# Performance work log

Hardware: AMD Instinct MI355X
Metric: run time of the kernel (lower is better)

Reference implementation:

```python
import jax, jax.numpy as jnp
import numpy as np

N = 10000        # nodes
E = 160000       # edges (before self-loops)
NFEAT = 256
NHID = 128
H = 4            # heads
NCLASS = 40
NLAYERS = 2
DT = 1.0
ALPHA = 1.0
GAMMA = 1.0
NEG_SLOPE = 0.2  # GATConv leaky_relu slope


def setup_inputs() -> dict:
    key = jax.random.key(0)
    ks = jax.random.split(key, 12)

    def glorot(k, shape):
        fan_in, fan_out = shape[-1], shape[0]
        lim = (6.0 / (fan_in + fan_out)) ** 0.5
        return jax.random.uniform(k, shape, jnp.float32, -lim, lim)

    return {
        "x": jax.random.normal(ks[0], (N, NFEAT), jnp.float32),
        "edge_index": jax.random.randint(ks[1], (2, E), 0, N, jnp.int64),
        "enc_w": glorot(ks[2], (NHID, NFEAT)),
        "enc_b": jnp.zeros((NHID,), jnp.float32),
        "res_w": glorot(ks[3], (H * NHID, NHID)),
        "res_b": jnp.zeros((H * NHID,), jnp.float32),
        "gat_w": glorot(ks[4], (H * NHID, NHID)),
        "att_src": glorot(ks[5], (H, NHID)) * 0.1,
        "att_dst": glorot(ks[6], (H, NHID)) * 0.1,
        "gat_b": jnp.zeros((H * NHID,), jnp.float32),
        "dec_w": glorot(ks[7], (NCLASS, NHID)),
        "dec_b": jnp.zeros((NCLASS,), jnp.float32),
    }


def _gat_conv(x, src, dst, gat_w, att_src, att_dst, gat_b):
    # x: [N, NHID] -> per-head features [N, H, C]
    xh = (x @ gat_w.T).reshape(N, H, NHID)
    a_src = jnp.sum(xh * att_src[None], axis=-1)  # [N, H]
    a_dst = jnp.sum(xh * att_dst[None], axis=-1)  # [N, H]
    e = jax.nn.leaky_relu(a_src[src] + a_dst[dst], NEG_SLOPE)  # [E', H]
    # segment softmax over incoming edges of each destination node
    m = jax.ops.segment_max(e, dst, num_segments=N)            # [N, H]
    e = jnp.exp(e - m[dst])
    s = jax.ops.segment_sum(e, dst, num_segments=N)            # [N, H]
    alpha = e / s[dst]                                          # [E', H]
    msg = xh[src] * alpha[:, :, None]                           # [E', H, C]
    out = jax.ops.segment_sum(msg, dst, num_segments=N)         # [N, H, C]
    return out.reshape(N, H * NHID) + gat_b


def reference(x, edge_index, enc_w, enc_b, res_w, res_b, gat_w,
              att_src, att_dst, gat_b, dec_w, dec_b):
    # add self-loops (GATConv default)
    loop = jnp.arange(N, dtype=edge_index.dtype)
    src = jnp.concatenate([edge_index[0], loop])
    dst = jnp.concatenate([edge_index[1], loop])

    Y = jax.nn.relu(x @ enc_w.T + enc_b)  # [N, NHID]
    X = Y
    for _ in range(NLAYERS):
        conv = _gat_conv(X, src, dst, gat_w, att_src, att_dst, gat_b)  # [N, H*NHID]
        res = X @ res_w.T + res_b                                       # [N, H*NHID]
        # faithful to .view(n_nodes, -1, nheads).mean(-1): [N, NHID, H] -> mean over heads axis
        z = jax.nn.elu(conv + res).reshape(N, NHID, H).mean(axis=-1)    # [N, NHID]
        Y = Y + DT * (z - ALPHA * Y - GAMMA * X)
        X = X + DT * Y
    return X @ dec_w.T + dec_b  # [N, NCLASS]
```

## Files before the change

### kernel.cpp

```cpp
#include <hip/hip_runtime.h>
#include <math.h>

#define NN 10000
#define EE 160000
#define EP 170000
#define NFEAT 256
#define NHID 128
#define NH 4
#define HF 512
#define NCLASS 40
#define FCOLS 1088

typedef __attribute__((ext_vector_type(8))) short bf8;
typedef __attribute__((ext_vector_type(8))) unsigned short u16x8;
typedef __attribute__((ext_vector_type(4))) float f4;

__device__ __forceinline__ float leaky02(float x) { return x >= 0.0f ? x : 0.2f * x; }

__device__ __forceinline__ unsigned short f2bf(float f) {
    unsigned u = __builtin_bit_cast(unsigned, f);
    unsigned r = (u + 0x7FFF + ((u >> 16) & 1)) >> 16;
    return (unsigned short)r;
}
__device__ __forceinline__ float bf2f(unsigned short h) {
    return __builtin_bit_cast(float, (unsigned)h << 16);
}

__device__ __forceinline__ int swz(int row, int c) {
    return ((((c >> 3) ^ (row & 7)) << 3) | (c & 7));
}

__device__ __forceinline__ void gl_lds16(const unsigned short* g, unsigned short* l)
{
    __builtin_amdgcn_global_load_lds(
        (const __attribute__((address_space(1))) unsigned int*)g,
        (__attribute__((address_space(3))) unsigned int*)l, 16, 0, 0);
}

#define C_X   2560000
#define C_EW  (C_X + 32768)
#define C_FW  (C_EW + 131072)
#define CVT_B  1330
#define ATTW_B (CVT_B + 8)
#define TOT_B  (ATTW_B + 166)

__global__ __launch_bounds__(256)
void fused0_k(const float* __restrict__ x, const float* __restrict__ enc_w,
              const float* __restrict__ gat_w, const float* __restrict__ res_w,
              const float* __restrict__ att_src, const float* __restrict__ att_dst,
              const float* __restrict__ res_b, const float* __restrict__ gat_b,
              const int* __restrict__ ei,
              unsigned short* __restrict__ xhi, unsigned short* __restrict__ ewhi,
              unsigned short* __restrict__ fwhi,
              float* __restrict__ biasRG, int* __restrict__ cnt)
{
    int bId = blockIdx.x;
    int t = threadIdx.x;
    if (bId < CVT_B) {
        int iu = bId * 256 + t;
        int i = iu * 8;
        const float* src = nullptr; unsigned short* ph; int j, row, c, Kd;
        if (i < C_X)       { j = i;        src = x;     ph = xhi;
                             row = j >> 8; c = j & 255; Kd = 256; }
        else if (i < C_EW) { j = i - C_X;  src = enc_w; ph = ewhi;
                             row = j >> 8; c = j & 255; Kd = 256; }
        else               { j = i - C_EW; ph = fwhi;
                             row = j >> 7; c = j & 127; Kd = 128; }
        float4 v0, v1;
        if (src) { v0 = *(const float4*)(src + j); v1 = *(const float4*)(src + j + 4); }
        else {
            const float* s2 = (j < 65536) ? (gat_w + j) : (res_w + j - 65536);
            v0 = *(const float4*)s2; v1 = *(const float4*)(s2 + 4);
        }
        float vv[8] = {v0.x, v0.y, v0.z, v0.w, v1.x, v1.y, v1.z, v1.w};
        unsigned short hs[8];
#pragma unroll
        for (int k = 0; k < 8; ++k) hs[k] = f2bf(vv[k]);
        int outp = row * Kd + swz(row, c);
        *(u16x8*)(ph + outp) = *(u16x8*)hs;
    } else if (bId < ATTW_B) {
        __shared__ float sm[256];
        int b = bId - CVT_B;
        int is_dst = b >> 2, h = b & 3;
        const float* att = is_dst ? att_dst : att_src;
        int k = t & 127, half = t >> 7;
        float s = 0.0f;
#pragma unroll 4
        for (int c = half * 64; c < half * 64 + 64; ++c)
            s = fmaf(gat_w[(size_t)(h * 128 + c) * 128 + k], att[h * 128 + c], s);
        sm[t] = s;
        __syncthreads();
        if (t < 128) {
            float v = sm[t] + sm[t + 128];
            int R = 1024 + is_dst * 4 + h;
            fwhi[(size_t)R * 128 + swz(R, k)] = f2bf(v);
        }
        for (int i = b * 896 + t; i < (b + 1) * 896; i += 256)
            fwhi[1032 * 128 + i] = 0;
        if (b < 2) {
            int c = b * 256 + t;
            biasRG[c] = res_b[c] + gat_b[c];
        }
    } else {
        for (int e = (bId - ATTW_B) * 256 + t; e < EP; e += (TOT_B - ATTW_B) * 256) {
            int d = (e < EE) ? ei[EE + e] : (e - EE);
            atomicAdd(&cnt[d], 1);
        }
    }
}

template<int MODE, int KTILES, int MERGE>
__global__ __launch_bounds__(256)
void gemm3_k(const unsigned short* __restrict__ A, const unsigned short* __restrict__ B,
             const float* __restrict__ bias,
             unsigned short* __restrict__ outH, unsigned short* __restrict__ outL,
             float* __restrict__ a_src, float* __restrict__ a_dst, int M,
             const int* __restrict__ ei, const int* __restrict__ cnt,
             int* __restrict__ row_ptr, int* __restrict__ cursor, int* __restrict__ csr)
{
    constexpr int K = KTILES * 128;
    __shared__ __align__(16) unsigned short smem[2 * 64 * 128];
    const int tid = threadIdx.x;

    if (MERGE && blockIdx.y == gridDim.y - 1) {
        if (MERGE == 1) {
            if (blockIdx.x != 0) return;
            int* smi = (int*)smem;
            int i0 = tid * 40, i1 = min(i0 + 40, NN);
            int part = 0;
            for (int i = i0; i < i1; ++i) part += cnt[i];
            smi[tid] = part;
            __syncthreads();
            for (int off = 1; off < 256; off <<= 1) {
                int v = (tid >= off) ? smi[tid - off] : 0;
                __syncthreads();
                smi[tid] += v;
                __syncthreads();
            }
            int run = smi[tid] - part;
            for (int i = i0; i < i1; ++i) { row_ptr[i] = run; run += cnt[i]; }
            if (tid == 255) row_ptr[NN] = run;
        } else {
            int stride = gridDim.x * 256;
            for (int e = blockIdx.x * 256 + tid; e < EP; e += stride) {
                int s, d;
                if (e < EE) { s = ei[e]; d = ei[EE + e]; } else { s = e - EE; d = s; }
                int pos = row_ptr[d] + atomicAdd(&cursor[d], 1);
                csr[pos] = s;
            }
        }
        return;
    }

    unsigned short* sA = smem;
    unsigned short* sB = smem + 8192;

    const int lane = tid & 63, wv = tid >> 6;
    const int wr = (wv >> 1) * 32, wc = (wv & 1) * 32;
    const int bm = blockIdx.x * 64, bn = blockIdx.y * 64;
    const int r16 = lane & 15, q4 = lane >> 4;

    f4 acc[2][2];
#pragma unroll
    for (int i = 0; i < 2; ++i)
#pragma unroll
        for (int j = 0; j < 2; ++j) acc[i][j] = (f4){0.f, 0.f, 0.f, 0.f};

    const int ra0 = wr + r16;
    const int rb0 = wc + r16;

    for (int kt = 0; kt < KTILES; ++kt) {
        if (kt) __syncthreads();
#pragma unroll
        for (int j = 0; j < 4; ++j) {
            int i = tid + j * 256;
            int row = i >> 4, u = i & 15;
            int arow = min(bm + row, M - 1);
            size_t ga = (size_t)arow * K + kt * 128 + u * 8;
            size_t gb = (size_t)(bn + row) * K + kt * 128 + u * 8;
            int lb = (wv * 64 + j * 256) * 8;
            gl_lds16(A + ga, sA + lb);
            gl_lds16(B + gb, sB + lb);
        }
        __syncthreads();

#pragma unroll
        for (int ks = 0; ks < 4; ++ks) {
            int u = ks * 4 + q4;
            int oa0 = ra0 * 128 + ((u ^ (ra0 & 7)) * 8);
            int ob0 = rb0 * 128 + ((u ^ (rb0 & 7)) * 8);
            int oa1 = oa0 + 16 * 128;
            int ob1 = ob0 + 16 * 128;
            bf8 A0 = *(const bf8*)(sA + oa0);
            bf8 A1 = *(const bf8*)(sA + oa1);
            bf8 B0 = *(const bf8*)(sB + ob0);
            bf8 B1 = *(const bf8*)(sB + ob1);

            acc[0][0] = __builtin_amdgcn_mfma_f32_16x16x32_bf16(A0, B0, acc[0][0], 0, 0, 0);
            acc[0][1] = __builtin_amdgcn_mfma_f32_16x16x32_bf16(A0, B1, acc[0][1], 0, 0, 0);
            acc[1][0] = __builtin_amdgcn_mfma_f32_16x16x32_bf16(A1, B0, acc[1][0], 0, 0, 0);
            acc[1][1] = __builtin_amdgcn_mfma_f32_16x16x32_bf16(A1, B1, acc[1][1], 0, 0, 0);
        }
    }

    const int rbase = q4 * 4;

    if (MODE == 2 && bn >= 1024) {
#pragma unroll
        for (int i = 0; i < 2; ++i)
#pragma unroll
            for (int j = 0; j < 2; ++j)
#pragma unroll
                for (int r = 0; r < 4; ++r) {
                    int row = bm + wr + i * 16 + rbase + r;
                    int col = bn + wc + j * 16 + r16;
                    if (row >= M || col >= 1032) continue;
                    float v = acc[i][j][r];
                    int h = col - 1024;
                    if (h < 4) a_src[row * 4 + h] = v;
                    else       a_dst[row * 4 + h - 4] = v;
                }
        return;
    }

    __syncthreads();
    float* sC = (float*)smem;
#pragma unroll
    for (int i = 0; i < 2; ++i)
#pragma unroll
        for (int j = 0; j < 2; ++j)
#pragma unroll
            for (int r = 0; r < 4; ++r)
                sC[(wr + i * 16 + rbase + r) * 65 + (wc + j * 16 + r16)] = acc[i][j][r];
    __syncthreads();

    int row = tid >> 2, seg = tid & 3, c0 = seg * 16;
    int grow = bm + row;
    if (grow < M) {
        float v[16];
#pragma unroll
        for (int k = 0; k < 16; ++k) v[k] = sC[row * 65 + c0 + k];

        if (MODE == 1) {
            unsigned short hs[16];
#pragma unroll
            for (int k = 0; k < 16; ++k)
                hs[k] = f2bf(fmaxf(v[k] + bias[bn + c0 + k], 0.0f));
#pragma unroll
            for (int uu = 0; uu < 2; ++uu) {
                int ug = (bn + c0) / 8 + uu;
                int pu = ug ^ (grow & 7);
                *(u16x8*)(outH + (size_t)grow * 128 + pu * 8) = *(u16x8*)(hs + uu * 8);
            }
        } else {
            if (bn < 512) {
                unsigned short hs[16];
#pragma unroll
                for (int k = 0; k < 16; ++k) hs[k] = f2bf(v[k]);
                *(u16x8*)(outH + (size_t)grow * 512 + bn + c0)     = *(u16x8*)hs;
                *(u16x8*)(outH + (size_t)grow * 512 + bn + c0 + 8) = *(u16x8*)(hs + 8);
            } else {
                unsigned short hs[16];
#pragma unroll
                for (int k = 0; k < 16; ++k) hs[k] = f2bf(v[k] + bias[bn - 512 + c0 + k]);
                *(u16x8*)(outL + (size_t)grow * 512 + (bn - 512) + c0)     = *(u16x8*)hs;
                *(u16x8*)(outL + (size_t)grow * 512 + (bn - 512) + c0 + 8) = *(u16x8*)(hs + 8);
            }
        }
    }
}

template<int DEC>
__global__ __launch_bounds__(256)
void agg_k(const int* __restrict__ row_ptr, const int* __restrict__ csr,
           const float* __restrict__ a_src, const float* __restrict__ a_dst,
           const unsigned short* __restrict__ xh_b, const unsigned short* __restrict__ resb,
           unsigned short* __restrict__ Xhi,
           const float* __restrict__ dec_w, const float* __restrict__ dec_b,
           float* __restrict__ out)
{
    __shared__ float sAcc[2][64][8];
    __shared__ float sSum[2][64];
    int tid = threadIdx.x;
    int wv = tid >> 6, lane = tid & 63;
    int pair = wv >> 1, half = wv & 1;
    int d = blockIdx.x * 2 + pair;
    int beg = row_ptr[d], end = row_ptr[d + 1];
    int len = end - beg;
    int h0 = (len + 1) >> 1;
    int eb = half ? (beg + h0) : beg;
    int en = half ? end : (beg + h0);
    int hl = lane >> 4;
    int cb = lane * 8;
    float ad = a_dst[d * 4 + hl];
    u16x8 rv = *(const u16x8*)(resb + (size_t)d * HF + cb);

    float acc[8];
#pragma unroll
    for (int k = 0; k < 8; ++k) acc[k] = 0.0f;
    float ssum = 0.0f;

    int e = eb;
    for (; e + 8 <= en; e += 8) {
        int sv[8]; float w[8]; u16x8 v[8];
#pragma unroll
        for (int q = 0; q < 8; ++q) sv[q] = csr[e + q];
#pragma unroll
        for (int q = 0; q < 8; ++q) v[q] = *(const u16x8*)(xh_b + (size_t)sv[q] * HF + cb);
#pragma unroll
        for (int q = 0; q < 8; ++q) {
            w[q] = __expf(leaky02(a_src[sv[q] * 4 + hl] + ad));
            ssum += w[q];
        }
#pragma unroll
        for (int q = 0; q < 8; ++q)
#pragma unroll
            for (int k = 0; k < 8; ++k) acc[k] = fmaf(w[q], bf2f(v[q][k]), acc[k]);
    }
    for (; e + 4 <= en; e += 4) {
        int sv[4]; float w[4]; u16x8 v[4];
#pragma unroll
        for (int q = 0; q < 4; ++q) sv[q] = csr[e + q];
#pragma unroll
        for (int q = 0; q < 4; ++q) v[q] = *(const u16x8*)(xh_b + (size_t)sv[q] * HF + cb);
#pragma unroll
        for (int q = 0; q < 4; ++q) {
            w[q] = __expf(leaky02(a_src[sv[q] * 4 + hl] + ad));
            ssum += w[q];
        }
#pragma unroll
        for (int q = 0; q < 4; ++q)
#pragma unroll
            for (int k = 0; k < 8; ++k) acc[k] = fmaf(w[q], bf2f(v[q][k]), acc[k]);
    }
    for (; e < en; ++e) {
        int s = csr[e];
        float w = __expf(leaky02(a_src[s * 4 + hl] + ad));
        ssum += w;
        u16x8 v = *(const u16x8*)(xh_b + (size_t)s * HF + cb);
#pragma unroll
        for (int k = 0; k < 8; ++k) acc[k] = fmaf(w, bf2f(v[k]), acc[k]);
    }

    if (half) {
        *(float4*)&sAcc[pair][lane][0] = make_float4(acc[0], acc[1], acc[2], acc[3]);
        *(float4*)&sAcc[pair][lane][4] = make_float4(acc[4], acc[5], acc[6], acc[7]);
        sSum[pair][lane] = ssum;
    }
    __syncthreads();

    float z0 = 0.0f, z1 = 0.0f;
    if (!half) {
#pragma unroll
        for (int k = 0; k < 8; ++k) acc[k] += sAcc[pair][lane][k];
        ssum += sSum[pair][lane];

        float inv = 1.0f / ssum;
        float uv[8];
#pragma unroll
        for (int k = 0; k < 8; ++k) {
            float v = fmaf(acc[k], inv, bf2f(rv[k]));
            uv[k] = (v > 0.0f) ? v : expm1f(v);
        }
        z0 = (uv[0] + uv[1] + uv[2] + uv[3]) * 0.25f;
        z1 = (uv[4] + uv[5] + uv[6] + uv[7]) * 0.25f;
        unsigned short h0b = f2bf(z0), h1b = f2bf(z1);
        int pos = swz(d, lane * 2);
        size_t idx = (size_t)d * NHID + pos;
        *(unsigned*)(Xhi + idx) = ((unsigned)h1b << 16) | h0b;
    }

    if (DEC) {
        __syncthreads();
        float* zbuf = &sAcc[0][0][0];
        if (!half) {
            zbuf[pair * 128 + lane * 2]     = z0;
            zbuf[pair * 128 + lane * 2 + 1] = z1;
        }
        __syncthreads();
        if (tid < 80) {
            int nd = tid >= 40;
            int cp = tid - nd * 40;
            const float* zr = zbuf + nd * 128;
            const float* wr = dec_w + cp * 128;
            float s = dec_b[cp];
#pragma unroll 8
            for (int c = 0; c < 128; ++c) s = fmaf(zr[c], wr[c], s);
            out[(size_t)(blockIdx.x * 2 + nd) * NCLASS + cp] = s;
        }
    }
}

extern "C" void kernel_launch(void* const* d_in, const int* in_sizes, int n_in,
                              void* d_out, int out_size, void* d_ws, size_t ws_size,
                              hipStream_t stream)
{
    const float* x       = (const float*)d_in[0];
    const int*   ei      = (const int*)d_in[1];
    const float* enc_w   = (const float*)d_in[2];
    const float* enc_b   = (const float*)d_in[3];
    const float* res_w   = (const float*)d_in[4];
    const float* res_b   = (const float*)d_in[5];
    const float* gat_w   = (const float*)d_in[6];
    const float* att_src = (const float*)d_in[7];
    const float* att_dst = (const float*)d_in[8];
    const float* gat_b   = (const float*)d_in[9];
    const float* dec_w   = (const float*)d_in[10];
    const float* dec_b   = (const float*)d_in[11];
    float* out = (float*)d_out;

    char* p = (char*)d_ws;
    auto alloc = [&](size_t bytes) -> void* {
        void* r = (void*)p;
        p += (bytes + 255) & ~(size_t)255;
        return r;
    };
    float* a_src  = (float*)alloc(40000 * 4);
    float* a_dst  = (float*)alloc(40000 * 4);
    float* biasRG = (float*)alloc(512 * 4);
    unsigned short* xh_b = (unsigned short*)alloc(5120000 * 2);
    unsigned short* resb = (unsigned short*)alloc(5120000 * 2);
    unsigned short* Xhi  = (unsigned short*)alloc(1280000 * 2);
    unsigned short* xhi  = (unsigned short*)alloc(2560000 * 2);
    unsigned short* ewhi = (unsigned short*)alloc(32768 * 2);
    unsigned short* fwhi = (unsigned short*)alloc(FCOLS * 128 * 2);
    int* row_ptr = (int*)alloc(10004 * 4);
    int* csr     = (int*)alloc(170000 * 4);
    char* zbase = p;
    int* cnt    = (int*)alloc(10000 * 4);
    int* cursor = (int*)alloc(10000 * 4);
    size_t zbytes = (size_t)(p - zbase);

    hipMemsetAsync(zbase, 0, zbytes, stream);

    fused0_k<<<TOT_B, 256, 0, stream>>>(
        x, enc_w, gat_w, res_w, att_src, att_dst, res_b, gat_b, ei,
        xhi, ewhi, fwhi, biasRG, cnt);

    gemm3_k<1, 2, 1><<<dim3(157, 3), 256, 0, stream>>>(
        xhi, ewhi, enc_b, Xhi, nullptr, nullptr, nullptr, NN,
        nullptr, cnt, row_ptr, nullptr, nullptr);

    gemm3_k<2, 1, 2><<<dim3(157, 18), 256, 0, stream>>>(
        Xhi, fwhi, biasRG, xh_b, resb, a_src, a_dst, NN,
        ei, nullptr, row_ptr, cursor, csr);
    agg_k<0><<<5000, 256, 0, stream>>>(row_ptr, csr, a_src, a_dst, xh_b, resb, Xhi,
                                       nullptr, nullptr, nullptr);

    gemm3_k<2, 1, 0><<<dim3(157, 17), 256, 0, stream>>>(
        Xhi, fwhi, biasRG, xh_b, resb, a_src, a_dst, NN,
        nullptr, nullptr, nullptr, nullptr, nullptr);
    agg_k<1><<<5000, 256, 0, stream>>>(row_ptr, csr, a_src, a_dst, xh_b, resb, Xhi,
                                       dec_w, dec_b, out);
}
```

Measured before the change: 223.3 us.

## Split aggregation per head across edge-groups and move decoder to MFMA GEMM

The aggregation kernel is reorganised so each block handles one head for four nodes: each wave's lanes cover four edge groups times 16 channel chunks, and the groups are combined with cross-lane shuffles instead of an LDS reduction between two half-waves. The decoder, previously a scalar per-block dot product fused into the last aggregation, becomes a separate bf16 MFMA GEMM launch reading a dec_w copy converted to bf16 in the prep kernel. This aims to remove block synchronisation and the slow scalar decode, at the cost of one extra launch and bf16 rounding of decoder weights. The same node's residual row and a_dst are now read by four different blocks, one per head.

Result: faster. 206.7 us (median of 2 runs) (-7.4%).

```diff
diff --git a/kernel.cpp b/kernel.cpp
--- a/kernel.cpp
+++ b/kernel.cpp
@@ -40,18 +40,20 @@
 #define C_X   2560000
 #define C_EW  (C_X + 32768)
 #define C_FW  (C_EW + 131072)
-#define CVT_B  1330
+#define C_DW  (C_FW + 5120)
+#define CVT_B  1333
 #define ATTW_B (CVT_B + 8)
 #define TOT_B  (ATTW_B + 166)
 
 __global__ __launch_bounds__(256)
 void fused0_k(const float* __restrict__ x, const float* __restrict__ enc_w,
               const float* __restrict__ gat_w, const float* __restrict__ res_w,
+              const float* __restrict__ dec_w,
               const float* __restrict__ att_src, const float* __restrict__ att_dst,
               const float* __restrict__ res_b, const float* __restrict__ gat_b,
               const int* __restrict__ ei,
               unsigned short* __restrict__ xhi, unsigned short* __restrict__ ewhi,
-              unsigned short* __restrict__ fwhi,
+              unsigned short* __restrict__ fwhi, unsigned short* __restrict__ dwhi,
               float* __restrict__ biasRG, int* __restrict__ cnt)
 {
     int bId = blockIdx.x;
@@ -59,12 +61,15 @@
     if (bId < CVT_B) {
         int iu = bId * 256 + t;
         int i = iu * 8;
+        if (i >= C_DW) return;
         const float* src = nullptr; unsigned short* ph; int j, row, c, Kd;
         if (i < C_X)       { j = i;        src = x;     ph = xhi;
                              row = j >> 8; c = j & 255; Kd = 256; }
         else if (i < C_EW) { j = i - C_X;  src = enc_w; ph = ewhi;
                              row = j >> 8; c = j & 255; Kd = 256; }
-        else               { j = i - C_EW; ph = fwhi;
+        else if (i < C_FW) { j = i - C_EW; ph = fwhi;
+                             row = j >> 7; c = j & 127; Kd = 128; }
+        else               { j = i - C_FW; src = dec_w; ph = dwhi;
                              row = j >> 7; c = j & 127; Kd = 128; }
         float4 v0, v1;
         if (src) { v0 = *(const float4*)(src + j); v1 = *(const float4*)(src + j + 4); }
@@ -112,7 +117,7 @@
 template<int MODE, int KTILES, int MERGE>
 __global__ __launch_bounds__(256)
 void gemm3_k(const unsigned short* __restrict__ A, const unsigned short* __restrict__ B,
-             const float* __restrict__ bias,
+             const float* __restrict__ bias, float* __restrict__ outF,
              unsigned short* __restrict__ outH, unsigned short* __restrict__ outL,
              float* __restrict__ a_src, float* __restrict__ a_dst, int M,
              const int* __restrict__ ei, const int* __restrict__ cnt,
@@ -205,7 +210,7 @@
 
     const int rbase = q4 * 4;
 
-    if (MODE == 2 && bn >= 1024) {
+    if (MODE == 0 || (MODE == 2 && bn >= 1024)) {
 #pragma unroll
         for (int i = 0; i < 2; ++i)
 #pragma unroll
@@ -214,11 +219,18 @@
                 for (int r = 0; r < 4; ++r) {
                     int row = bm + wr + i * 16 + rbase + r;
                     int col = bn + wc + j * 16 + r16;
-                    if (row >= M || col >= 1032) continue;
+                    if (row >= M) continue;
                     float v = acc[i][j][r];
-                    int h = col - 1024;
-                    if (h < 4) a_src[row * 4 + h] = v;
-                    else       a_dst[row * 4 + h - 4] = v;
+                    if (MODE == 0) {
+                        if (col < NCLASS)
+                            outF[(size_t)row * NCLASS + col] = v + bias[col];
+                    } else {
+                        if (col < 1032) {
+                            int h = col - 1024;
+                            if (h < 4) a_src[row * 4 + h] = v;
+                            else       a_dst[row * 4 + h - 4] = v;
+                        }
+                    }
                 }
         return;
     }
@@ -270,29 +282,21 @@
     }
 }
 
-template<int DEC>
 __global__ __launch_bounds__(256)
 void agg_k(const int* __restrict__ row_ptr, const int* __restrict__ csr,
            const float* __restrict__ a_src, const float* __restrict__ a_dst,
            const unsigned short* __restrict__ xh_b, const unsigned short* __restrict__ resb,
-           unsigned short* __restrict__ Xhi,
-           const float* __restrict__ dec_w, const float* __restrict__ dec_b,
-           float* __restrict__ out)
+           unsigned short* __restrict__ Xhi)
 {
-    __shared__ float sAcc[2][64][8];
-    __shared__ float sSum[2][64];
-    int tid = threadIdx.x;
-    int wv = tid >> 6, lane = tid & 63;
-    int pair = wv >> 1, half = wv & 1;
-    int d = blockIdx.x * 2 + pair;
+    int bx = blockIdx.x;
+    int h  = bx / 2500;
+    int ng = bx - h * 2500;
+    int wv = threadIdx.x >> 6, lane = threadIdx.x & 63;
+    int d = ng * 4 + wv;
     int beg = row_ptr[d], end = row_ptr[d + 1];
-    int len = end - beg;
-    int h0 = (len + 1) >> 1;
-    int eb = half ? (beg + h0) : beg;
-    int en = half ? end : (beg + h0);
-    int hl = lane >> 4;
-    int cb = lane * 8;
-    float ad = a_dst[d * 4 + hl];
+    int eg = lane >> 4, c16 = lane & 15;
+    int cb = h * 128 + c16 * 8;
+    float ad = a_dst[d * 4 + h];
     u16x8 rv = *(const u16x8*)(resb + (size_t)d * HF + cb);
 
     float acc[8];
@@ -300,94 +304,61 @@
     for (int k = 0; k < 8; ++k) acc[k] = 0.0f;
     float ssum = 0.0f;
 
-    int e = eb;
-    for (; e + 8 <= en; e += 8) {
-        int sv[8]; float w[8]; u16x8 v[8];
-#pragma unroll
-        for (int q = 0; q < 8; ++q) sv[q] = csr[e + q];
-#pragma unroll
-        for (int q = 0; q < 8; ++q) v[q] = *(const u16x8*)(xh_b + (size_t)sv[q] * HF + cb);
-#pragma unroll
-        for (int q = 0; q < 8; ++q) {
-            w[q] = __expf(leaky02(a_src[sv[q] * 4 + hl] + ad));
+    int e = beg;
+    for (; e + 16 <= end; e += 16) {
+        int sv[4]; float w[4]; u16x8 v[4];
+#pragma unroll
+        for (int q = 0; q < 4; ++q) sv[q] = csr[e + q * 4 + eg];
+#pragma unroll
+        for (int q = 0; q < 4; ++q) v[q] = *(const u16x8*)(xh_b + (size_t)sv[q] * HF + cb);
+#pragma unroll
+        for (int q = 0; q < 4; ++q) {
+            w[q] = __expf(leaky02(a_src[sv[q] * 4 + h] + ad));
             ssum += w[q];
         }
 #pragma unroll
-        for (int q = 0; q < 8; ++q)
+        for (int q = 0; q < 4; ++q)
 #pragma unroll
             for (int k = 0; k < 8; ++k) acc[k] = fmaf(w[q], bf2f(v[q][k]), acc[k]);
     }
-    for (; e + 4 <= en; e += 4) {
-        int sv[4]; float w[4]; u16x8 v[4];
-#pragma unroll
-        for (int q = 0; q < 4; ++q) sv[q] = csr[e + q];
-#pragma unroll
-        for (int q = 0; q < 4; ++q) v[q] = *(const u16x8*)(xh_b + (size_t)sv[q] * HF + cb);
-#pragma unroll
-        for (int q = 0; q < 4; ++q) {
-            w[q] = __expf(leaky02(a_src[sv[q] * 4 + hl] + ad));
-            ssum += w[q];
-        }
-#pragma unroll
-        for (int q = 0; q < 4; ++q)
-#pragma unroll
-            for (int k = 0; k < 8; ++k) acc[k] = fmaf(w[q], bf2f(v[q][k]), acc[k]);
-    }
-    for (; e < en; ++e) {
-        int s = csr[e];
-        float w = __expf(leaky02(a_src[s * 4 + hl] + ad));
+    for (; e + 4 <= end; e += 4) {
+        int s = csr[e + eg];
+        u16x8 v = *(const u16x8*)(xh_b + (size_t)s * HF + cb);
+        float w = __expf(leaky02(a_src[s * 4 + h] + ad));
         ssum += w;
+#pragma unroll
+        for (int k = 0; k < 8; ++k) acc[k] = fmaf(w, bf2f(v[k]), acc[k]);
+    }
+    if (e + eg < end) {
+        int s = csr[e + eg];
         u16x8 v = *(const u16x8*)(xh_b + (size_t)s * HF + cb);
+        float w = __expf(leaky02(a_src[s * 4 + h] + ad));
+        ssum += w;
 #pragma unroll
         for (int k = 0; k < 8; ++k) acc[k] = fmaf(w, bf2f(v[k]), acc[k]);
     }
 
-    if (half) {
-        *(float4*)&sAcc[pair][lane][0] = make_float4(acc[0], acc[1], acc[2], acc[3]);
-        *(float4*)&sAcc[pair][lane][4] = make_float4(acc[4], acc[5], acc[6], acc[7]);
-        sSum[pair][lane] = ssum;
-    }
-    __syncthreads();
-
-    float z0 = 0.0f, z1 = 0.0f;
-    if (!half) {
-#pragma unroll
-        for (int k = 0; k < 8; ++k) acc[k] += sAcc[pair][lane][k];
-        ssum += sSum[pair][lane];
-
-        float inv = 1.0f / ssum;
-        float uv[8];
-#pragma unroll
-        for (int k = 0; k < 8; ++k) {
-            float v = fmaf(acc[k], inv, bf2f(rv[k]));
-            uv[k] = (v > 0.0f) ? v : expm1f(v);
-        }
-        z0 = (uv[0] + uv[1] + uv[2] + uv[3]) * 0.25f;
-        z1 = (uv[4] + uv[5] + uv[6] + uv[7]) * 0.25f;
+#pragma unroll
+    for (int off = 16; off <= 32; off <<= 1) {
+        ssum += __shfl_xor(ssum, off);
+#pragma unroll
+        for (int k = 0; k < 8; ++k) acc[k] += __shfl_xor(acc[k], off);
+    }
+
+    float inv = 1.0f / ssum;
+    float uv[8];
+#pragma unroll
+    for (int k = 0; k < 8; ++k) {
+        float v = fmaf(acc[k], inv, bf2f(rv[k]));
+        uv[k] = (v > 0.0f) ? v : expm1f(v);
+    }
+    float z0 = (uv[0] + uv[1] + uv[2] + uv[3]) * 0.25f;
+    float z1 = (uv[4] + uv[5] + uv[6] + uv[7]) * 0.25f;
+    if (eg == 0) {
+        int col = h * 32 + c16 * 2;
         unsigned short h0b = f2bf(z0), h1b = f2bf(z1);
-        int pos = swz(d, lane * 2);
-        size_t idx = (size_t)d * NHID + pos;
+        size_t idx = (size_t)d * NHID + swz(d, col);
         *(unsigned*)(Xhi + idx) = ((unsigned)h1b << 16) | h0b;
-    }
-
-    if (DEC) {
-        __syncthreads();
-        float* zbuf = &sAcc[0][0][0];
-        if (!half) {
-            zbuf[pair * 128 + lane * 2]     = z0;
-            zbuf[pair * 128 + lane * 2 + 1] = z1;
-        }
-        __syncthreads();
-        if (tid < 80) {
-            int nd = tid >= 40;
-            int cp = tid - nd * 40;
-            const float* zr = zbuf + nd * 128;
-            const float* wr = dec_w + cp * 128;
-            float s = dec_b[cp];
-#pragma unroll 8
-            for (int c = 0; c < 128; ++c) s = fmaf(zr[c], wr[c], s);
-            out[(size_t)(blockIdx.x * 2 + nd) * NCLASS + cp] = s;
-        }
     }
 }
 
@@ -427,6 +398,7 @@
     int* row_ptr = (int*)alloc(10004 * 4);
     int* csr     = (int*)alloc(170000 * 4);
     char* zbase = p;
+    unsigned short* dwhi = (unsigned short*)alloc(8192 * 2);
     int* cnt    = (int*)alloc(10000 * 4);
     int* cursor = (int*)alloc(10000 * 4);
     size_t zbytes = (size_t)(p - zbase);
@@ -434,22 +406,24 @@
     hipMemsetAsync(zbase, 0, zbytes, stream);
 
     fused0_k<<<TOT_B, 256, 0, stream>>>(
-        x, enc_w, gat_w, res_w, att_src, att_dst, res_b, gat_b, ei,
-        xhi, ewhi, fwhi, biasRG, cnt);
+        x, enc_w, gat_w, res_w, dec_w, att_src, att_dst, res_b, gat_b, ei,
+        xhi, ewhi, fwhi, dwhi, biasRG, cnt);
 
     gemm3_k<1, 2, 1><<<dim3(157, 3), 256, 0, stream>>>(
-        xhi, ewhi, enc_b, Xhi, nullptr, nullptr, nullptr, NN,
+        xhi, ewhi, enc_b, nullptr, Xhi, nullptr, nullptr, nullptr, NN,
         nullptr, cnt, row_ptr, nullptr, nullptr);
 
     gemm3_k<2, 1, 2><<<dim3(157, 18), 256, 0, stream>>>(
-        Xhi, fwhi, biasRG, xh_b, resb, a_src, a_dst, NN,
+        Xhi, fwhi, biasRG, nullptr, xh_b, resb, a_src, a_dst, NN,
         ei, nullptr, row_ptr, cursor, csr);
-    agg_k<0><<<5000, 256, 0, stream>>>(row_ptr, csr, a_src, a_dst, xh_b, resb, Xhi,
-                                       nullptr, nullptr, nullptr);
+    agg_k<<<10000, 256, 0, stream>>>(row_ptr, csr, a_src, a_dst, xh_b, resb, Xhi);
 
     gemm3_k<2, 1, 0><<<dim3(157, 17), 256, 0, stream>>>(
-        Xhi, fwhi, biasRG, xh_b, resb, a_src, a_dst, NN,
+        Xhi, fwhi, biasRG, nullptr, xh_b, resb, a_src, a_dst, NN,
         nullptr, nullptr, nullptr, nullptr, nullptr);
-    agg_k<1><<<5000, 256, 0, stream>>>(row_ptr, csr, a_src, a_dst, xh_b, resb, Xhi,
-                                       dec_w, dec_b, out);
-}
+    agg_k<<<10000, 256, 0, stream>>>(row_ptr, csr, a_src, a_dst, xh_b, resb, Xhi);
+
+    gemm3_k<0, 1, 0><<<dim3(157, 1), 256, 0, stream>>>(
+        Xhi, dwhi, dec_b, out, nullptr, nullptr, nullptr, nullptr, NN,
+        nullptr, nullptr, nullptr, nullptr, nullptr);
+}
```
